# Kernel tuning notes

Measured on AMD Instinct MI355X. Metric: run time of the kernel, lower is better.

## Reference

```python
import jax, jax.numpy as jnp
import numpy as np

EPS = 1e-12

def _l2norm(v):
    return v / jnp.maximum(jnp.linalg.norm(v), EPS)

def setup_inputs() -> dict:
    key = jax.random.key(0)
    k1, k2, k3, k4 = jax.random.split(key, 4)
    B, C, H, Wd = 32, 64, 128, 128
    x = jax.random.normal(k1, (B, C, H, Wd), dtype=jnp.float32)
    W = jax.random.normal(k2, (C, C), dtype=jnp.float32)
    gamma = jax.random.uniform(k3, (1,), dtype=jnp.float32)
    u = jax.random.normal(k4, (C,), dtype=jnp.float32)
    return {"x": x, "W": W, "gamma": gamma, "u": u}

def reference(x, W, gamma, u):
    # --- spectral norm: one power iteration (u is the stored buffer) ---
    v = _l2norm(W.T @ u)          # [C]
    u2 = _l2norm(W @ v)           # [C]
    sigma = u2 @ (W @ v)          # scalar, largest singular value estimate
    Wsn = W / sigma               # ks=1 conv weight, normalized

    B, C = x.shape[0], x.shape[1]
    xf = x.reshape(B, C, -1)                        # [B,C,N]
    convx = jnp.einsum('oc,bcn->bon', Wsn, xf)      # 1x1 conv
    xxT = jnp.einsum('bcn,bdn->bcd', xf, xf)        # Gram [B,C,C]
    o = jnp.einsum('bcd,bdn->bcn', xxT, convx)      # [B,C,N]
    out = gamma[0] * o + xf
    return out.reshape(x.shape)
```

## Files before the change

### kernel.cpp

```cpp
#include <hip/hip_runtime.h>

#define NN 16384
#define CC 64
#define BB 32

typedef __attribute__((ext_vector_type(8))) short bf16x8;
typedef __attribute__((ext_vector_type(4))) float f32x4;
typedef __attribute__((ext_vector_type(16))) float f32x16;

__device__ __forceinline__ unsigned short f2bf(float f) {
    unsigned int u = __float_as_uint(f);
    unsigned int r = (u + 0x7fffu + ((u >> 16) & 1u)) >> 16;
    return (unsigned short)r;
}

__device__ __forceinline__ bf16x8 cvt8(float4 a, float4 b) {
    union { bf16x8 v; unsigned short s[8]; } u;
    u.s[0] = f2bf(a.x); u.s[1] = f2bf(a.y); u.s[2] = f2bf(a.z); u.s[3] = f2bf(a.w);
    u.s[4] = f2bf(b.x); u.s[5] = f2bf(b.y); u.s[6] = f2bf(b.z); u.s[7] = f2bf(b.w);
    return u.v;
}

__global__ __launch_bounds__(64) void k_sigma(const float* __restrict__ W,
                                              const float* __restrict__ u,
                                              float* __restrict__ Wsn) {
    __shared__ float sv[64];
    int c = threadIdx.x;
    float t = 0.f;
    for (int r = 0; r < 64; ++r) t += W[r * 64 + c] * u[r];
    float s = t * t;
    #pragma unroll
    for (int m = 1; m < 64; m <<= 1) s += __shfl_xor(s, m);
    float nv = sqrtf(s);
    float v = t / fmaxf(nv, 1e-12f);
    sv[c] = v;
    __syncthreads();
    float wv = 0.f;
    for (int k = 0; k < 64; ++k) wv += W[c * 64 + k] * sv[k];
    float s2 = wv * wv;
    #pragma unroll
    for (int m = 1; m < 64; m <<= 1) s2 += __shfl_xor(s2, m);
    float nw = sqrtf(s2);
    float sigma = s2 / fmaxf(nw, 1e-12f);
    float inv = 1.0f / fmaxf(sigma, 1e-30f);
    for (int i = c; i < 4096; i += 64) Wsn[i] = W[i] * inv;
}

__global__ __launch_bounds__(256) void k_gram(const float* __restrict__ x,
                                              float* __restrict__ G) {
    const int S = 16;
    int b = blockIdx.x / S, chunk = blockIdx.x % S;
    int wave = threadIdx.x >> 6, lane = threadIdx.x & 63;
    int lrow = lane & 15, quad = lane >> 4;
    const float* xb = x + (size_t)b * CC * NN;
    int kbase = chunk * (NN / S) + wave * (NN / S / 4);

    f32x4 acc[4][4] = {};
    for (int ks = 0; ks < 8; ++ks) {
        int k0 = kbase + ks * 32 + quad * 8;
        bf16x8 fr[4];
        #pragma unroll
        for (int ti = 0; ti < 4; ++ti) {
            const float* p = xb + (size_t)(16 * ti + lrow) * NN + k0;
            float4 a  = *(const float4*)p;
            float4 b4 = *(const float4*)(p + 4);
            fr[ti] = cvt8(a, b4);
        }
        #pragma unroll
        for (int mi = 0; mi < 4; ++mi)
            #pragma unroll
            for (int ni = 0; ni < 4; ++ni)
                acc[mi][ni] = __builtin_amdgcn_mfma_f32_16x16x32_bf16(
                    fr[mi], fr[ni], acc[mi][ni], 0, 0, 0);
    }

    __shared__ float Gs[4096];
    for (int w = 0; w < 4; ++w) {
        if (wave == w) {
            #pragma unroll
            for (int mi = 0; mi < 4; ++mi)
                #pragma unroll
                for (int ni = 0; ni < 4; ++ni)
                    #pragma unroll
                    for (int r = 0; r < 4; ++r) {
                        int row = 16 * mi + quad * 4 + r;
                        int col = 16 * ni + lrow;
                        if (w == 0) Gs[row * 64 + col]  = acc[mi][ni][r];
                        else        Gs[row * 64 + col] += acc[mi][ni][r];
                    }
        }
        __syncthreads();
    }
    float* Gb = G + b * 4096;
    for (int i = threadIdx.x; i < 4096; i += 256) atomicAdd(&Gb[i], Gs[i]);
}

__global__ __launch_bounds__(256) void k_build_A(const float* __restrict__ G,
                                                 const float* __restrict__ Wsn,
                                                 const float* __restrict__ gamma,
                                                 unsigned short* __restrict__ Afrag) {
    int b = blockIdx.x;
    __shared__ float Gs[4096], Ws[4096], As[4096];
    for (int i = threadIdx.x; i < 4096; i += 256) {
        Gs[i] = G[b * 4096 + i];
        Ws[i] = Wsn[i];
    }
    __syncthreads();
    float g = gamma[0];
    for (int i = threadIdx.x; i < 4096; i += 256) {
        int r = i >> 6, c = i & 63;
        float a = 0.f;
        #pragma unroll 8
        for (int k = 0; k < 64; ++k) a += Gs[r * 64 + k] * Ws[k * 64 + c];
        a *= g;
        if (r == c) a += 1.f;
        As[i] = a;
    }
    __syncthreads();
    unsigned short* Ab = Afrag + b * 4096;
    for (int fi = threadIdx.x; fi < 4096; fi += 256) {
        int j = fi & 7, lane = (fi >> 3) & 63, mi = (fi >> 9) & 1, ks = fi >> 10;
        int row = 32 * mi + (lane & 31);
        int col = ks * 16 + (lane >> 5) * 8 + j;
        Ab[fi] = f2bf(As[row * 64 + col]);
    }
}

#define PITCH 72
__global__ __launch_bounds__(256) void k_out(const float* __restrict__ x,
                                             const unsigned short* __restrict__ Afrag,
                                             float* __restrict__ out) {
    int nblk = blockIdx.x & 127;
    int b = blockIdx.x >> 7;
    int col0 = nblk * 128;
    int wave = threadIdx.x >> 6, lane = threadIdx.x & 63;
    const float* xb = x + (size_t)b * CC * NN;

    __shared__ unsigned short XT[128 * PITCH];

    {
        int p  = threadIdx.x >> 3;
        int cs = (threadIdx.x & 7) * 16;
        int r0 = p * 2;
        const float* pr0 = xb + (size_t)r0 * NN + col0 + cs;
        const float* pr1 = pr0 + NN;
        #pragma unroll
        for (int q = 0; q < 4; ++q) {
            float4 a  = *(const float4*)(pr0 + q * 4);
            float4 b4 = *(const float4*)(pr1 + q * 4);
            const float* av = (const float*)&a;
            const float* bv = (const float*)&b4;
            #pragma unroll
            for (int e = 0; e < 4; ++e) {
                int n = cs + q * 4 + e;
                unsigned int lo = f2bf(av[e]);
                unsigned int hi = f2bf(bv[e]);
                *(unsigned int*)&XT[n * PITCH + r0] = lo | (hi << 16);
            }
        }
    }

    bf16x8 af[4][2];
    const unsigned short* Ab = Afrag + (size_t)b * 4096;
    #pragma unroll
    for (int ks = 0; ks < 4; ++ks)
        #pragma unroll
        for (int mi = 0; mi < 2; ++mi)
            af[ks][mi] = *(const bf16x8*)(Ab + ((ks * 2 + mi) * 64 + lane) * 8);

    __syncthreads();

    f32x16 acc[2] = {};
    int n = wave * 32 + (lane & 31);
    int khalf = (lane >> 5) * 8;
    #pragma unroll
    for (int ks = 0; ks < 4; ++ks) {
        bf16x8 bf = *(const bf16x8*)&XT[n * PITCH + ks * 16 + khalf];
        acc[0] = __builtin_amdgcn_mfma_f32_32x32x16_bf16(af[ks][0], bf, acc[0], 0, 0, 0);
        acc[1] = __builtin_amdgcn_mfma_f32_32x32x16_bf16(af[ks][1], bf, acc[1], 0, 0, 0);
    }

    float* ob = out + (size_t)b * CC * NN;
    int gcol = col0 + n;
    #pragma unroll
    for (int mi = 0; mi < 2; ++mi)
        #pragma unroll
        for (int r = 0; r < 16; ++r) {
            int grow = 32 * mi + (r & 3) + 8 * (r >> 2) + 4 * (lane >> 5);
            ob[(size_t)grow * NN + gcol] = acc[mi][r];
        }
}

extern "C" void kernel_launch(void* const* d_in, const int* in_sizes, int n_in,
                              void* d_out, int out_size, void* d_ws, size_t ws_size,
                              hipStream_t stream) {
    const float* x     = (const float*)d_in[0];
    const float* W     = (const float*)d_in[1];
    const float* gamma = (const float*)d_in[2];
    const float* u     = (const float*)d_in[3];
    float* out = (float*)d_out;

    char* ws = (char*)d_ws;
    float* Wsn            = (float*)ws;
    float* G              = (float*)(ws + 16 * 1024);
    unsigned short* Afrag = (unsigned short*)(ws + 528 * 1024);

    hipMemsetAsync(G, 0, (size_t)BB * 4096 * sizeof(float), stream);
    k_sigma<<<1, 64, 0, stream>>>(W, u, Wsn);
    k_gram<<<BB * 16, 256, 0, stream>>>(x, G);
    k_build_A<<<BB, 256, 0, stream>>>(G, Wsn, gamma, Afrag);
    k_out<<<BB * 128, 256, 0, stream>>>(x, Afrag, out);
}
```

Measured before the change: 283.3 us.

## Fuse sigma into build_A, replace Gram atomics with partials, retune LDS pitches

Removes the separate sigma kernel and the memset, folding the power iteration into k_build_A, which now also scales by gamma/sigma. k_gram switches to 8 chunks of 512 threads that write per-chunk partial Gram matrices instead of atomically adding into global memory. k_build_A sums those partials and computes the 64x64 product with register tiling and vectorized LDS reads and bf16 packing. k_out changes its LDS pitch and transpose thread mapping and splits the B-fragment read into two 8-byte loads, aiming to reduce bank conflicts. The goal is fewer launches and less atomic and serialized-LDS overhead, at the cost of more workspace traffic for the partials and a larger LDS footprint in k_gram.

Measured after the change: 278.5 us. About the same (-1.7%).

```diff
diff --git a/kernel.cpp b/kernel.cpp
--- a/kernel.cpp
+++ b/kernel.cpp
@@ -5,6 +5,7 @@
 #define BB 32
 
 typedef __attribute__((ext_vector_type(8))) short bf16x8;
+typedef __attribute__((ext_vector_type(4))) short bf16x4;
 typedef __attribute__((ext_vector_type(4))) float f32x4;
 typedef __attribute__((ext_vector_type(16))) float f32x16;
 
@@ -21,39 +22,16 @@
     return u.v;
 }
 
-__global__ __launch_bounds__(64) void k_sigma(const float* __restrict__ W,
-                                              const float* __restrict__ u,
-                                              float* __restrict__ Wsn) {
-    __shared__ float sv[64];
-    int c = threadIdx.x;
-    float t = 0.f;
-    for (int r = 0; r < 64; ++r) t += W[r * 64 + c] * u[r];
-    float s = t * t;
-    #pragma unroll
-    for (int m = 1; m < 64; m <<= 1) s += __shfl_xor(s, m);
-    float nv = sqrtf(s);
-    float v = t / fmaxf(nv, 1e-12f);
-    sv[c] = v;
-    __syncthreads();
-    float wv = 0.f;
-    for (int k = 0; k < 64; ++k) wv += W[c * 64 + k] * sv[k];
-    float s2 = wv * wv;
-    #pragma unroll
-    for (int m = 1; m < 64; m <<= 1) s2 += __shfl_xor(s2, m);
-    float nw = sqrtf(s2);
-    float sigma = s2 / fmaxf(nw, 1e-12f);
-    float inv = 1.0f / fmaxf(sigma, 1e-30f);
-    for (int i = c; i < 4096; i += 64) Wsn[i] = W[i] * inv;
-}
-
-__global__ __launch_bounds__(256) void k_gram(const float* __restrict__ x,
-                                              float* __restrict__ G) {
-    const int S = 16;
-    int b = blockIdx.x / S, chunk = blockIdx.x % S;
+#define GP 68
+__global__ __launch_bounds__(512) void k_gram(const float* __restrict__ x,
+                                              float* __restrict__ Gp) {
+    int b = blockIdx.x >> 3, chunk = blockIdx.x & 7;
     int wave = threadIdx.x >> 6, lane = threadIdx.x & 63;
     int lrow = lane & 15, quad = lane >> 4;
     const float* xb = x + (size_t)b * CC * NN;
-    int kbase = chunk * (NN / S) + wave * (NN / S / 4);
+    int kbase = chunk * 2048 + wave * 256;
+
+    __shared__ float Gw[8 * 64 * GP];
 
     f32x4 acc[4][4] = {};
     for (int ks = 0; ks < 8; ++ks) {
@@ -74,59 +52,113 @@
                     fr[mi], fr[ni], acc[mi][ni], 0, 0, 0);
     }
 
-    __shared__ float Gs[4096];
-    for (int w = 0; w < 4; ++w) {
-        if (wave == w) {
+    float* gw = Gw + wave * 64 * GP;
+    #pragma unroll
+    for (int mi = 0; mi < 4; ++mi)
+        #pragma unroll
+        for (int ni = 0; ni < 4; ++ni)
             #pragma unroll
-            for (int mi = 0; mi < 4; ++mi)
-                #pragma unroll
-                for (int ni = 0; ni < 4; ++ni)
-                    #pragma unroll
-                    for (int r = 0; r < 4; ++r) {
-                        int row = 16 * mi + quad * 4 + r;
-                        int col = 16 * ni + lrow;
-                        if (w == 0) Gs[row * 64 + col]  = acc[mi][ni][r];
-                        else        Gs[row * 64 + col] += acc[mi][ni][r];
-                    }
-        }
-        __syncthreads();
-    }
-    float* Gb = G + b * 4096;
-    for (int i = threadIdx.x; i < 4096; i += 256) atomicAdd(&Gb[i], Gs[i]);
-}
-
-__global__ __launch_bounds__(256) void k_build_A(const float* __restrict__ G,
-                                                 const float* __restrict__ Wsn,
+            for (int r = 0; r < 4; ++r) {
+                int row = 16 * mi + quad * 4 + r;
+                int col = 16 * ni + lrow;
+                gw[row * GP + col] = acc[mi][ni][r];
+            }
+    __syncthreads();
+
+    float* gp = Gp + ((size_t)b * 8 + chunk) * 4096;
+    for (int i = threadIdx.x; i < 4096; i += 512) {
+        int off = (i >> 6) * GP + (i & 63);
+        float s = 0.f;
+        #pragma unroll
+        for (int w = 0; w < 8; ++w) s += Gw[w * 64 * GP + off];
+        gp[i] = s;
+    }
+}
+
+__global__ __launch_bounds__(256) void k_build_A(const float* __restrict__ W,
+                                                 const float* __restrict__ u,
                                                  const float* __restrict__ gamma,
+                                                 const float* __restrict__ Gp,
                                                  unsigned short* __restrict__ Afrag) {
     int b = blockIdx.x;
-    __shared__ float Gs[4096], Ws[4096], As[4096];
-    for (int i = threadIdx.x; i < 4096; i += 256) {
-        Gs[i] = G[b * 4096 + i];
-        Ws[i] = Wsn[i];
-    }
-    __syncthreads();
-    float g = gamma[0];
-    for (int i = threadIdx.x; i < 4096; i += 256) {
-        int r = i >> 6, c = i & 63;
-        float a = 0.f;
+    int tid = threadIdx.x;
+    __shared__ float Ws[4096];
+    __shared__ float Gs[64 * 65];
+    __shared__ float As[64 * 68];
+    __shared__ float us[64];
+    __shared__ float gshare;
+
+    for (int i = tid; i < 4096; i += 256) Ws[i] = W[i];
+    if (tid < 64) us[tid] = u[tid];
+    __syncthreads();
+
+    if (tid < 64) {
+        int c = tid;
+        float t = 0.f;
         #pragma unroll 8
-        for (int k = 0; k < 64; ++k) a += Gs[r * 64 + k] * Ws[k * 64 + c];
-        a *= g;
-        if (r == c) a += 1.f;
-        As[i] = a;
-    }
-    __syncthreads();
-    unsigned short* Ab = Afrag + b * 4096;
-    for (int fi = threadIdx.x; fi < 4096; fi += 256) {
-        int j = fi & 7, lane = (fi >> 3) & 63, mi = (fi >> 9) & 1, ks = fi >> 10;
+        for (int r = 0; r < 64; ++r) t += Ws[r * 64 + c] * us[r];
+        float s = t * t;
+        #pragma unroll
+        for (int m = 1; m < 64; m <<= 1) s += __shfl_xor(s, m);
+        float v = t / fmaxf(sqrtf(s), 1e-12f);
+        float wv = 0.f;
+        #pragma unroll 8
+        for (int k = 0; k < 64; ++k) wv += Ws[c * 64 + k] * __shfl(v, k);
+        float s2 = wv * wv;
+        #pragma unroll
+        for (int m = 1; m < 64; m <<= 1) s2 += __shfl_xor(s2, m);
+        float nw = sqrtf(s2);
+        float sigma = s2 / fmaxf(nw, 1e-12f);
+        if (c == 0) gshare = gamma[0] / fmaxf(sigma, 1e-30f);
+    }
+
+    const float* gp = Gp + (size_t)b * 8 * 4096;
+    for (int i = tid; i < 4096; i += 256) {
+        float s = 0.f;
+        #pragma unroll
+        for (int c = 0; c < 8; ++c) s += gp[c * 4096 + i];
+        Gs[(i >> 6) * 65 + (i & 63)] = s;
+    }
+    __syncthreads();
+
+    {
+        int r = tid >> 2, j0 = (tid & 3) * 16;
+        float a[16];
+        #pragma unroll
+        for (int j = 0; j < 16; ++j) a[j] = 0.f;
+        for (int k = 0; k < 64; ++k) {
+            float g = Gs[r * 65 + k];
+            const float* wr = &Ws[k * 64 + j0];
+            float4 w0 = *(const float4*)(wr);
+            float4 w1 = *(const float4*)(wr + 4);
+            float4 w2 = *(const float4*)(wr + 8);
+            float4 w3 = *(const float4*)(wr + 12);
+            a[0]  += g * w0.x; a[1]  += g * w0.y; a[2]  += g * w0.z; a[3]  += g * w0.w;
+            a[4]  += g * w1.x; a[5]  += g * w1.y; a[6]  += g * w1.z; a[7]  += g * w1.w;
+            a[8]  += g * w2.x; a[9]  += g * w2.y; a[10] += g * w2.z; a[11] += g * w2.w;
+            a[12] += g * w3.x; a[13] += g * w3.y; a[14] += g * w3.z; a[15] += g * w3.w;
+        }
+        float g2 = gshare;
+        #pragma unroll
+        for (int j = 0; j < 16; ++j) {
+            float vv = a[j] * g2 + ((r == j0 + j) ? 1.f : 0.f);
+            As[r * 68 + j0 + j] = vv;
+        }
+    }
+    __syncthreads();
+
+    unsigned short* Ab = Afrag + (size_t)b * 4096;
+    for (int fv = tid; fv < 512; fv += 256) {
+        int ks = fv >> 7, mi = (fv >> 6) & 1, lane = fv & 63;
         int row = 32 * mi + (lane & 31);
-        int col = ks * 16 + (lane >> 5) * 8 + j;
-        Ab[fi] = f2bf(As[row * 64 + col]);
-    }
-}
-
-#define PITCH 72
+        int col = 16 * ks + (lane >> 5) * 8;
+        float4 a4 = *(const float4*)&As[row * 68 + col];
+        float4 b4 = *(const float4*)&As[row * 68 + col + 4];
+        *(bf16x8*)(Ab + (size_t)fv * 8) = cvt8(a4, b4);
+    }
+}
+
+#define PITCH 68
 __global__ __launch_bounds__(256) void k_out(const float* __restrict__ x,
                                              const unsigned short* __restrict__ Afrag,
                                              float* __restrict__ out) {
@@ -136,12 +168,13 @@
     int wave = threadIdx.x >> 6, lane = threadIdx.x & 63;
     const float* xb = x + (size_t)b * CC * NN;
 
-    __shared__ unsigned short XT[128 * PITCH];
+    __shared__ __align__(16) unsigned short XT[128 * PITCH];
 
     {
-        int p  = threadIdx.x >> 3;
-        int cs = (threadIdx.x & 7) * 16;
-        int r0 = p * 2;
+        int rp = threadIdx.x & 31;
+        int nc = threadIdx.x >> 5;
+        int r0 = rp * 2;
+        int cs = nc * 16;
         const float* pr0 = xb + (size_t)r0 * NN + col0 + cs;
         const float* pr1 = pr0 + NN;
         #pragma unroll
@@ -172,12 +205,14 @@
 
     f32x16 acc[2] = {};
     int n = wave * 32 + (lane & 31);
-    int khalf = (lane >> 5) * 8;
+    int kh = (lane >> 5) * 8;
     #pragma unroll
     for (int ks = 0; ks < 4; ++ks) {
-        bf16x8 bf = *(const bf16x8*)&XT[n * PITCH + ks * 16 + khalf];
-        acc[0] = __builtin_amdgcn_mfma_f32_32x32x16_bf16(af[ks][0], bf, acc[0], 0, 0, 0);
-        acc[1] = __builtin_amdgcn_mfma_f32_32x32x16_bf16(af[ks][1], bf, acc[1], 0, 0, 0);
+        union { bf16x8 v; bf16x4 h[2]; } bu;
+        bu.h[0] = *(const bf16x4*)&XT[n * PITCH + ks * 16 + kh];
+        bu.h[1] = *(const bf16x4*)&XT[n * PITCH + ks * 16 + kh + 4];
+        acc[0] = __builtin_amdgcn_mfma_f32_32x32x16_bf16(af[ks][0], bu.v, acc[0], 0, 0, 0);
+        acc[1] = __builtin_amdgcn_mfma_f32_32x32x16_bf16(af[ks][1], bu.v, acc[1], 0, 0, 0);
     }
 
     float* ob = out + (size_t)b * CC * NN;
@@ -201,13 +236,10 @@
     float* out = (float*)d_out;
 
     char* ws = (char*)d_ws;
-    float* Wsn            = (float*)ws;
-    float* G              = (float*)(ws + 16 * 1024);
-    unsigned short* Afrag = (unsigned short*)(ws + 528 * 1024);
-
-    hipMemsetAsync(G, 0, (size_t)BB * 4096 * sizeof(float), stream);
-    k_sigma<<<1, 64, 0, stream>>>(W, u, Wsn);
-    k_gram<<<BB * 16, 256, 0, stream>>>(x, G);
-    k_build_A<<<BB, 256, 0, stream>>>(G, Wsn, gamma, Afrag);
+    float* Gp             = (float*)ws;
+    unsigned short* Afrag = (unsigned short*)(ws + (5 << 20));
+
+    k_gram<<<BB * 8, 512, 0, stream>>>(x, Gp);
+    k_build_A<<<BB, 256, 0, stream>>>(W, u, gamma, Gp, Afrag);
     k_out<<<BB * 128, 256, 0, stream>>>(x, Afrag, out);
 }
```
